# Optimization experiments

Measured on AMD Instinct MI355X. Metric: run time of the kernel, lower is better.

## Reference

```python
import jax, jax.numpy as jnp
import numpy as np

N, E = 50000, 1600000
IN_CH, TOTAL_OUT, HEADS, NUM_LAYERS = 128, 64, 4, 3
C = TOTAL_OUT // HEADS  # out channels per head = 16
NEG_SLOPE = 0.2


def setup_inputs() -> dict:
    key = jax.random.key(0)
    ks = jax.random.split(key, 20)
    inp = {
        'x': jax.random.normal(ks[0], (N, IN_CH), dtype=jnp.float32),
        'edge_index': jax.random.randint(ks[1], (2, E), 0, N, dtype=jnp.int64),
    }
    ki = 2
    for i in range(NUM_LAYERS):
        fan_in = IN_CH if i == 0 else TOTAL_OUT
        s = 1.0 / np.sqrt(fan_in)
        inp[f'W{i}'] = jax.random.uniform(ks[ki], (fan_in, HEADS * C), jnp.float32, -s, s); ki += 1
        inp[f'att_src{i}'] = jax.random.uniform(ks[ki], (HEADS, C), jnp.float32, -s, s); ki += 1
        inp[f'att_dst{i}'] = jax.random.uniform(ks[ki], (HEADS, C), jnp.float32, -s, s); ki += 1
        inp[f'b{i}'] = jnp.zeros((HEADS * C,), dtype=jnp.float32)
    return inp


def gat_layer(x, src, dst, W, att_src, att_dst, b):
    n = x.shape[0]
    h = (x @ W).reshape(n, HEADS, C)                      # [N,H,C]
    a_s = (h * att_src).sum(-1)                            # [N,H]
    a_d = (h * att_dst).sum(-1)                            # [N,H]
    e = jax.nn.leaky_relu(a_s[src] + a_d[dst], NEG_SLOPE)  # [E',H]
    # segment softmax over incoming edges of each dst node
    m = jax.ops.segment_max(e, dst, num_segments=n)        # [N,H]
    ex = jnp.exp(e - m[dst])
    denom = jax.ops.segment_sum(ex, dst, num_segments=n)   # [N,H]
    alpha = ex / (denom[dst] + 1e-16)                      # [E',H]
    out = jax.ops.segment_sum(h[src] * alpha[:, :, None], dst, num_segments=n)  # [N,H,C]
    return out.reshape(n, HEADS * C) + b


def reference(x, edge_index, W0, att_src0, att_dst0, b0,
              W1, att_src1, att_dst1, b1,
              W2, att_src2, att_dst2, b2) -> jnp.ndarray:
    n = x.shape[0]
    loop = jnp.arange(n, dtype=edge_index.dtype)
    src = jnp.concatenate([edge_index[0], loop])  # add_self_loops=True (PyG default)
    dst = jnp.concatenate([edge_index[1], loop])
    params = [(W0, att_src0, att_dst0, b0), (W1, att_src1, att_dst1, b1), (W2, att_src2, att_dst2, b2)]
    h = x
    for i, (W, a_s, a_d, b) in enumerate(params):
        h = gat_layer(h, src, dst, W, a_s, a_d, b)
        if i < NUM_LAYERS - 1:
            h = jax.nn.relu(h)
    return h
```

## Files before the change

### kernel.cpp

```cpp
#include <hip/hip_runtime.h>
#include <hip/hip_fp16.h>
#include <math.h>

#define NN 50000
#define EE 1600000
#define HEADS 4
#define OUTC 64
#define NEG_SLOPE 0.2f

#define BM 64
#define BK 64

#define NB 196
#define RECTOT (EE + NN)
#define PCHUNK 4096
#define SEGCAP 12288
#define BINCAP 9500


__global__ void initcsr_kernel(int* __restrict__ fill1, int* __restrict__ rowptr) {
    int t = threadIdx.x;
    if (t < NB) fill1[t] = 0;
    if (t == 0) rowptr[NN] = RECTOT;
}

__global__ __launch_bounds__(256) void partition_kernel(
        const int* __restrict__ src, const int* __restrict__ dst,
        int* __restrict__ fill1, unsigned* __restrict__ bucket) {
    __shared__ int bh[NB], bbase[NB];
    int t = threadIdx.x;
    if (t < NB) bh[t] = 0;
    __syncthreads();
    int base = blockIdx.x * PCHUNK;
    int dv[16], sv[16], lr[16];
    #pragma unroll
    for (int j = 0; j < 16; ++j) {
        int i = base + j * 256 + t;
        bool valid = i < RECTOT;
        int d = -1, s = 0;
        if (valid) {
            if (i < EE) { d = dst[i]; s = src[i]; }
            else        { d = i - EE; s = d; }
        }
        dv[j] = d; sv[j] = s;
        lr[j] = valid ? atomicAdd(&bh[d >> 8], 1) : 0;
    }
    __syncthreads();
    if (t < NB && bh[t]) bbase[t] = atomicAdd(&fill1[t], bh[t]);
    __syncthreads();
    #pragma unroll
    for (int j = 0; j < 16; ++j) {
        if (dv[j] >= 0) {
            int bin = dv[j] >> 8;
            int pos = bbase[bin] + lr[j];
            if (pos < BINCAP)
                bucket[(size_t)bin * BINCAP + pos] =
                    ((unsigned)(dv[j] & 255) << 16) | (unsigned)sv[j];
        }
    }
}

__global__ void scan_hi_kernel(const int* __restrict__ fill1, int* __restrict__ binStart) {
    int t = threadIdx.x, lane = t & 63, w = t >> 6;
    __shared__ int wsum[4];
    int v = (t < NB) ? fill1[t] : 0;
    int s = v;
    #pragma unroll
    for (int off = 1; off < 64; off <<= 1) {
        int u = __shfl_up(s, off);
        if (lane >= off) s += u;
    }
    if (lane == 63) wsum[w] = s;
    __syncthreads();
    int add = 0;
    for (int i = 0; i < w; ++i) add += wsum[i];
    int excl = add + s - v;
    if (t <= NB) binStart[t] = excl;
}

__global__ __launch_bounds__(256) void seg_sort_kernel(
        const unsigned* __restrict__ bucket, const int* __restrict__ binStart,
        int* __restrict__ rowptr, unsigned short* __restrict__ col) {
    __shared__ unsigned stage[SEGCAP];
    __shared__ int h2[256], b2[256], c2[256];
    __shared__ int wsum[4];
    int t = threadIdx.x, lane = t & 63, w = t >> 6;
    int b = blockIdx.x;
    int segbase = binStart[b], segend = binStart[b + 1];
    int len = segend - segbase;
    const unsigned* __restrict__ bin = bucket + (size_t)b * BINCAP;
    h2[t] = 0; c2[t] = 0;
    __syncthreads();
    for (int i = t; i < len; i += 256) {
        unsigned r = bin[i];
        stage[i] = r;
        atomicAdd(&h2[(r >> 16) & 255], 1);
    }
    __syncthreads();
    int v = h2[t], s = v;
    #pragma unroll
    for (int off = 1; off < 64; off <<= 1) {
        int u = __shfl_up(s, off);
        if (lane >= off) s += u;
    }
    if (lane == 63) wsum[w] = s;
    __syncthreads();
    int add = 0;
    for (int i = 0; i < w; ++i) add += wsum[i];
    int excl = add + s - v;
    b2[t] = excl;
    int d = (b << 8) + t;
    if (d < NN) rowptr[d] = segbase + excl;
    __syncthreads();
    for (int i = t; i < len; i += 256) {
        unsigned r = stage[i];
        int low = (r >> 16) & 255;
        int pos = b2[low] + atomicAdd(&c2[low], 1);
        col[segbase + pos] = (unsigned short)(r & 0xFFFFu);
    }
}

__global__ __launch_bounds__(256) void gemm_att_kernel(
        const float* __restrict__ x, const float* __restrict__ W,
        const float* __restrict__ att_src, const float* __restrict__ att_dst,
        __half* __restrict__ h16,
        float* __restrict__ a_s, float* __restrict__ a_d,
        int n, int K) {
    __shared__ float Xt[BK][BM + 4];
    __shared__ float Ws[BK][OUTC + 4];
    int tid = (int)threadIdx.x;
    int tx = tid & 15, ty = tid >> 4;
    int row0 = blockIdx.x * BM;

    float acc[4][4] = {};

    for (int k0 = 0; k0 < K; k0 += BK) {
        {
            int rb = tid >> 4;
            int kb = tid & 15;
            float4 v0, v1, v2, v3;
            {
                int r0 = row0 + 4 * rb;
                int ra = r0 + 0; if (ra >= n) ra = n - 1;
                int rbx = r0 + 1; if (rbx >= n) rbx = n - 1;
                int rc = r0 + 2; if (rc >= n) rc = n - 1;
                int rd = r0 + 3; if (rd >= n) rd = n - 1;
                const float* xb = x + (size_t)k0 + 4 * kb;
                v0 = *(const float4*)(xb + (size_t)ra * K);
                v1 = *(const float4*)(xb + (size_t)rbx * K);
                v2 = *(const float4*)(xb + (size_t)rc * K);
                v3 = *(const float4*)(xb + (size_t)rd * K);
            }
            *(float4*)&Xt[4 * kb + 0][4 * rb] = make_float4(v0.x, v1.x, v2.x, v3.x);
            *(float4*)&Xt[4 * kb + 1][4 * rb] = make_float4(v0.y, v1.y, v2.y, v3.y);
            *(float4*)&Xt[4 * kb + 2][4 * rb] = make_float4(v0.z, v1.z, v2.z, v3.z);
            *(float4*)&Xt[4 * kb + 3][4 * rb] = make_float4(v0.w, v1.w, v2.w, v3.w);
        }
        {
            int k = tid >> 2;
            int c = (tid & 3) * 16;
            const float4* wp = (const float4*)(W + (size_t)(k0 + k) * OUTC + c);
            float4 v0 = wp[0], v1 = wp[1], v2 = wp[2], v3 = wp[3];
            *(float4*)&Ws[k][c]      = v0;
            *(float4*)&Ws[k][c + 4]  = v1;
            *(float4*)&Ws[k][c + 8]  = v2;
            *(float4*)&Ws[k][c + 12] = v3;
        }
        __syncthreads();
        #pragma unroll 8
        for (int k = 0; k < BK; ++k) {
            float4 xv = *(const float4*)&Xt[k][ty * 4];
            float4 wv = *(const float4*)&Ws[k][tx * 4];
            acc[0][0] = fmaf(xv.x, wv.x, acc[0][0]); acc[0][1] = fmaf(xv.x, wv.y, acc[0][1]);
            acc[0][2] = fmaf(xv.x, wv.z, acc[0][2]); acc[0][3] = fmaf(xv.x, wv.w, acc[0][3]);
            acc[1][0] = fmaf(xv.y, wv.x, acc[1][0]); acc[1][1] = fmaf(xv.y, wv.y, acc[1][1]);
            acc[1][2] = fmaf(xv.y, wv.z, acc[1][2]); acc[1][3] = fmaf(xv.y, wv.w, acc[1][3]);
            acc[2][0] = fmaf(xv.z, wv.x, acc[2][0]); acc[2][1] = fmaf(xv.z, wv.y, acc[2][1]);
            acc[2][2] = fmaf(xv.z, wv.z, acc[2][2]); acc[2][3] = fmaf(xv.z, wv.w, acc[2][3]);
            acc[3][0] = fmaf(xv.w, wv.x, acc[3][0]); acc[3][1] = fmaf(xv.w, wv.y, acc[3][1]);
            acc[3][2] = fmaf(xv.w, wv.z, acc[3][2]); acc[3][3] = fmaf(xv.w, wv.w, acc[3][3]);
        }
        __syncthreads();
    }

    float as0 = att_src[tx * 4 + 0], as1 = att_src[tx * 4 + 1];
    float as2 = att_src[tx * 4 + 2], as3 = att_src[tx * 4 + 3];
    float ad0 = att_dst[tx * 4 + 0], ad1 = att_dst[tx * 4 + 1];
    float ad2 = att_dst[tx * 4 + 2], ad3 = att_dst[tx * 4 + 3];
    int head = tx >> 2;
    #pragma unroll
    for (int i = 0; i < 4; ++i) {
        int row = row0 + ty * 4 + i;
        bool ok = row < n;
        if (ok) {
            union { __half2 h2[2]; uint2 u; } pk;
            pk.h2[0] = __floats2half2_rn(acc[i][0], acc[i][1]);
            pk.h2[1] = __floats2half2_rn(acc[i][2], acc[i][3]);
            *(uint2*)(h16 + (size_t)row * OUTC + tx * 4) = pk.u;
        }
        float ps = acc[i][0] * as0 + acc[i][1] * as1 + acc[i][2] * as2 + acc[i][3] * as3;
        float pd = acc[i][0] * ad0 + acc[i][1] * ad1 + acc[i][2] * ad2 + acc[i][3] * ad3;
        ps += __shfl_xor(ps, 1); ps += __shfl_xor(ps, 2);
        pd += __shfl_xor(pd, 1); pd += __shfl_xor(pd, 2);
        if (ok && (tx & 3) == 0) {
            a_s[row * HEADS + head] = ps;
            a_d[row * HEADS + head] = pd;
        }
    }
}

__global__ __launch_bounds__(256) void gat_aggr16_kernel(
        const int* __restrict__ rowptr, const unsigned short* __restrict__ col,
        const __half* __restrict__ h16, const float* __restrict__ a_s,
        const float* __restrict__ a_d, const float* __restrict__ bias,
        float* __restrict__ out, int n, int do_relu) {
    int node = __builtin_amdgcn_readfirstlane(
        (int)((blockIdx.x * 256u + threadIdx.x) >> 6));
    if (node >= n) return;
    int lane = (int)(threadIdx.x & 63);
    int slot = lane >> 4;
    int cl   = lane & 15;
    int head = cl >> 2;

    int beg = rowptr[node], end = rowptr[node + 1];
    float ad_h = a_d[(node << 2) | head];
    const uint2* __restrict__ hp = (const uint2*)h16;

    float4 acc = make_float4(0.f, 0.f, 0.f, 0.f);
    float den = 0.f;
    int e = beg + slot;
    for (; e + 4 < end; e += 8) {
        int s0 = (int)col[e], s1 = (int)col[e + 4];
        float as0 = a_s[(s0 << 2) | head];
        float as1 = a_s[(s1 << 2) | head];
        uint2 r0 = hp[(s0 << 4) | cl];
        uint2 r1 = hp[(s1 << 4) | cl];
        union { uint2 u; __half2 h2[2]; } p0, p1;
        p0.u = r0; p1.u = r1;
        float2 f00 = __half22float2(p0.h2[0]), f01 = __half22float2(p0.h2[1]);
        float2 f10 = __half22float2(p1.h2[0]), f11 = __half22float2(p1.h2[1]);
        float x0 = as0 + ad_h; x0 = fmaxf(x0, NEG_SLOPE * x0);
        float x1 = as1 + ad_h; x1 = fmaxf(x1, NEG_SLOPE * x1);
        float e0 = __expf(x0), e1 = __expf(x1);
        acc.x = fmaf(e0, f00.x, acc.x); acc.y = fmaf(e0, f00.y, acc.y);
        acc.z = fmaf(e0, f01.x, acc.z); acc.w = fmaf(e0, f01.y, acc.w);
        acc.x = fmaf(e1, f10.x, acc.x); acc.y = fmaf(e1, f10.y, acc.y);
        acc.z = fmaf(e1, f11.x, acc.z); acc.w = fmaf(e1, f11.y, acc.w);
        den += e0 + e1;
    }
    for (; e < end; e += 4) {
        int s0 = (int)col[e];
        float as0 = a_s[(s0 << 2) | head];
        uint2 r0 = hp[(s0 << 4) | cl];
        union { uint2 u; __half2 h2[2]; } p0;
        p0.u = r0;
        float2 f00 = __half22float2(p0.h2[0]), f01 = __half22float2(p0.h2[1]);
        float x0 = as0 + ad_h; x0 = fmaxf(x0, NEG_SLOPE * x0);
        float e0 = __expf(x0);
        acc.x = fmaf(e0, f00.x, acc.x); acc.y = fmaf(e0, f00.y, acc.y);
        acc.z = fmaf(e0, f01.x, acc.z); acc.w = fmaf(e0, f01.y, acc.w);
        den += e0;
    }
    acc.x += __shfl_xor(acc.x, 16); acc.y += __shfl_xor(acc.y, 16);
    acc.z += __shfl_xor(acc.z, 16); acc.w += __shfl_xor(acc.w, 16);
    den   += __shfl_xor(den, 16);
    acc.x += __shfl_xor(acc.x, 32); acc.y += __shfl_xor(acc.y, 32);
    acc.z += __shfl_xor(acc.z, 32); acc.w += __shfl_xor(acc.w, 32);
    den   += __shfl_xor(den, 32);
    if (slot == 0) {
        float inv = 1.0f / (den + 1e-16f);
        float4 bv = ((const float4*)bias)[cl];
        float rx = fmaf(acc.x, inv, bv.x);
        float ry = fmaf(acc.y, inv, bv.y);
        float rz = fmaf(acc.z, inv, bv.z);
        float rw = fmaf(acc.w, inv, bv.w);
        if (do_relu) {
            rx = fmaxf(rx, 0.f); ry = fmaxf(ry, 0.f);
            rz = fmaxf(rz, 0.f); rw = fmaxf(rw, 0.f);
        }
        ((float4*)out)[(node << 4) | cl] = make_float4(rx, ry, rz, rw);
    }
}

extern "C" void kernel_launch(void* const* d_in, const int* in_sizes, int n_in,
                              void* d_out, int out_size, void* d_ws, size_t ws_size,
                              hipStream_t stream) {
    const float* x  = (const float*)d_in[0];
    const int*   ei = (const int*)d_in[1];
    const int*   srcv = ei;
    const int*   dstv = ei + EE;

    const float* W[3]  = { (const float*)d_in[2], (const float*)d_in[6],  (const float*)d_in[10] };
    const float* AS[3] = { (const float*)d_in[3], (const float*)d_in[7],  (const float*)d_in[11] };
    const float* AD[3] = { (const float*)d_in[4], (const float*)d_in[8],  (const float*)d_in[12] };
    const float* B[3]  = { (const float*)d_in[5], (const float*)d_in[9],  (const float*)d_in[13] };

    char* ws = (char*)d_ws;
    size_t off = 0;
    auto carve = [&](size_t bytes) -> char* {
        char* p = ws + off;
        off = (off + bytes + 255) & ~(size_t)255;
        return p;
    };
    int*            rowptr   = (int*)carve((NN + 1) * sizeof(int));
    int*            fill1    = (int*)carve(NB * sizeof(int));
    int*            binStart = (int*)carve((NB + 1) * sizeof(int));
    unsigned short* colv     = (unsigned short*)carve((size_t)RECTOT * sizeof(unsigned short));
    size_t regionA_bytes = (size_t)NB * BINCAP * sizeof(unsigned);
    char*     regionA = carve(regionA_bytes);
    unsigned* bucket  = (unsigned*)regionA;
    __half*   h16     = (__half*)regionA;
    float* xbuf     = (float*)carve((size_t)NN * OUTC * sizeof(float));
    float* a_s      = (float*)carve((size_t)NN * HEADS * sizeof(float));
    float* a_d      = (float*)carve((size_t)NN * HEADS * sizeof(float));

    int pgrid = (RECTOT + PCHUNK - 1) / PCHUNK;
    initcsr_kernel<<<1, 256, 0, stream>>>(fill1, rowptr);
    partition_kernel<<<pgrid, 256, 0, stream>>>(srcv, dstv, fill1, bucket);
    scan_hi_kernel<<<1, 256, 0, stream>>>(fill1, binStart);
    seg_sort_kernel<<<NB, 256, 0, stream>>>(bucket, binStart, rowptr, colv);

    int grid_gemm = (NN + BM - 1) / BM;
    int grid_aggr = (NN + 3) / 4;

    gemm_att_kernel<<<grid_gemm, 256, 0, stream>>>(x, W[0], AS[0], AD[0],
                                                   h16, a_s, a_d, NN, 128);
    gat_aggr16_kernel<<<grid_aggr, 256, 0, stream>>>(rowptr, colv, h16, a_s, a_d, B[0], xbuf, NN, 1);
    gemm_att_kernel<<<grid_gemm, 256, 0, stream>>>(xbuf, W[1], AS[1], AD[1],
                                                   h16, a_s, a_d, NN, 64);
    gat_aggr16_kernel<<<grid_aggr, 256, 0, stream>>>(rowptr, colv, h16, a_s, a_d, B[1], xbuf, NN, 1);
    gemm_att_kernel<<<grid_gemm, 256, 0, stream>>>(xbuf, W[2], AS[2], AD[2],
                                                   h16, a_s, a_d, NN, 64);
    gat_aggr16_kernel<<<grid_aggr, 256, 0, stream>>>(rowptr, colv, h16, a_s, a_d, B[2], (float*)d_out, NN, 0);
}
```

Measured before the change: 212.9 us.

## Co-schedule CSR build with layer-0 GEMM and widen aggregation loads to 16B

The CSR partition and segment-sort kernels now share launches with halves of the layer-0 GEMM, so independent graph-preprocessing and GEMM blocks run concurrently. To allow this, the bucket buffer and h16 no longer alias in workspace. The init kernel becomes a memset, and the rowptr sentinel write moves into the scan. The aggregation kernel now uses 8 lanes per edge with 16-byte loads instead of 16 lanes with 8-byte loads, which processes 8 edges per wave-iteration and adds a third reduction step. The costs are more workspace memory and higher register and shared-memory footprint in the fused kernels.

```diff
diff --git a/kernel.cpp b/kernel.cpp
--- a/kernel.cpp
+++ b/kernel.cpp
@@ -14,24 +14,21 @@
 #define NB 196
 #define RECTOT (EE + NN)
 #define PCHUNK 4096
-#define SEGCAP 12288
+#define PGRID ((RECTOT + PCHUNK - 1) / PCHUNK)
 #define BINCAP 9500
-
-
-__global__ void initcsr_kernel(int* __restrict__ fill1, int* __restrict__ rowptr) {
-    int t = threadIdx.x;
-    if (t < NB) fill1[t] = 0;
-    if (t == 0) rowptr[NN] = RECTOT;
-}
-
-__global__ __launch_bounds__(256) void partition_kernel(
+#define GEMM_BLKS 782
+#define GEMM_A 391
+#define GEMM_B 391
+
+
+__device__ __forceinline__ void partition_body(
+        int* bh, int* bbase, int blk,
         const int* __restrict__ src, const int* __restrict__ dst,
         int* __restrict__ fill1, unsigned* __restrict__ bucket) {
-    __shared__ int bh[NB], bbase[NB];
-    int t = threadIdx.x;
+    int t = (int)threadIdx.x;
     if (t < NB) bh[t] = 0;
     __syncthreads();
-    int base = blockIdx.x * PCHUNK;
+    int base = blk * PCHUNK;
     int dv[16], sv[16], lr[16];
     #pragma unroll
     for (int j = 0; j < 16; ++j) {
@@ -60,32 +57,16 @@
     }
 }
 
-__global__ void scan_hi_kernel(const int* __restrict__ fill1, int* __restrict__ binStart) {
-    int t = threadIdx.x, lane = t & 63, w = t >> 6;
-    __shared__ int wsum[4];
-    int v = (t < NB) ? fill1[t] : 0;
-    int s = v;
-    #pragma unroll
-    for (int off = 1; off < 64; off <<= 1) {
-        int u = __shfl_up(s, off);
-        if (lane >= off) s += u;
-    }
-    if (lane == 63) wsum[w] = s;
-    __syncthreads();
-    int add = 0;
-    for (int i = 0; i < w; ++i) add += wsum[i];
-    int excl = add + s - v;
-    if (t <= NB) binStart[t] = excl;
-}
-
-__global__ __launch_bounds__(256) void seg_sort_kernel(
+__device__ __forceinline__ void seg_sort_body(
+        unsigned char* smem, int b,
         const unsigned* __restrict__ bucket, const int* __restrict__ binStart,
         int* __restrict__ rowptr, unsigned short* __restrict__ col) {
-    __shared__ unsigned stage[SEGCAP];
-    __shared__ int h2[256], b2[256], c2[256];
-    __shared__ int wsum[4];
-    int t = threadIdx.x, lane = t & 63, w = t >> 6;
-    int b = blockIdx.x;
+    unsigned* stage = (unsigned*)smem;
+    int* h2   = (int*)(smem + 38016);
+    int* b2   = h2 + 256;
+    int* c2   = b2 + 256;
+    int* wsum = c2 + 256;
+    int t = (int)threadIdx.x, lane = t & 63, w = t >> 6;
     int segbase = binStart[b], segend = binStart[b + 1];
     int len = segend - segbase;
     const unsigned* __restrict__ bin = bucket + (size_t)b * BINCAP;
@@ -120,17 +101,16 @@
     }
 }
 
-__global__ __launch_bounds__(256) void gemm_att_kernel(
+__device__ __forceinline__ void gemm_body(
+        float (*Xt)[BM + 4], float (*Ws)[OUTC + 4], int gblk,
         const float* __restrict__ x, const float* __restrict__ W,
         const float* __restrict__ att_src, const float* __restrict__ att_dst,
         __half* __restrict__ h16,
         float* __restrict__ a_s, float* __restrict__ a_d,
         int n, int K) {
-    __shared__ float Xt[BK][BM + 4];
-    __shared__ float Ws[BK][OUTC + 4];
     int tid = (int)threadIdx.x;
     int tx = tid & 15, ty = tid >> 4;
-    int row0 = blockIdx.x * BM;
+    int row0 = gblk * BM;
 
     float acc[4][4] = {};
 
@@ -209,6 +189,70 @@
     }
 }
 
+
+__global__ __launch_bounds__(256) void fused_part_gemm(
+        const int* __restrict__ src, const int* __restrict__ dst,
+        int* __restrict__ fill1, unsigned* __restrict__ bucket,
+        const float* __restrict__ x, const float* __restrict__ W,
+        const float* __restrict__ att_src, const float* __restrict__ att_dst,
+        __half* __restrict__ h16, float* __restrict__ a_s, float* __restrict__ a_d,
+        int n, int K) {
+    __shared__ float Xt[BK][BM + 4];
+    __shared__ float Ws[BK][OUTC + 4];
+    __shared__ int bh[NB], bbase[NB];
+    int b = (int)blockIdx.x;
+    if (b < PGRID) partition_body(bh, bbase, b, src, dst, fill1, bucket);
+    else           gemm_body(Xt, Ws, b - PGRID, x, W, att_src, att_dst, h16, a_s, a_d, n, K);
+}
+
+__global__ void scan_hi_kernel(const int* __restrict__ fill1, int* __restrict__ binStart,
+                               int* __restrict__ rowptr) {
+    int t = threadIdx.x, lane = t & 63, w = t >> 6;
+    __shared__ int wsum[4];
+    int v = (t < NB) ? fill1[t] : 0;
+    int s = v;
+    #pragma unroll
+    for (int off = 1; off < 64; off <<= 1) {
+        int u = __shfl_up(s, off);
+        if (lane >= off) s += u;
+    }
+    if (lane == 63) wsum[w] = s;
+    __syncthreads();
+    int add = 0;
+    for (int i = 0; i < w; ++i) add += wsum[i];
+    int excl = add + s - v;
+    if (t <= NB) binStart[t] = excl;
+    if (t == 0) rowptr[NN] = RECTOT;
+}
+
+__global__ __launch_bounds__(256) void fused_sort_gemm(
+        const unsigned* __restrict__ bucket, const int* __restrict__ binStart,
+        int* __restrict__ rowptr, unsigned short* __restrict__ col,
+        const float* __restrict__ x, const float* __restrict__ W,
+        const float* __restrict__ att_src, const float* __restrict__ att_dst,
+        __half* __restrict__ h16, float* __restrict__ a_s, float* __restrict__ a_d,
+        int n, int K) {
+    __shared__ __align__(16) unsigned char smem[41216];
+    int b = (int)blockIdx.x;
+    if (b < NB) {
+        seg_sort_body(smem, b, bucket, binStart, rowptr, col);
+    } else {
+        float (*Xt)[BM + 4]   = (float(*)[BM + 4])smem;
+        float (*Ws)[OUTC + 4] = (float(*)[OUTC + 4])(smem + sizeof(float) * BK * (BM + 4));
+        gemm_body(Xt, Ws, GEMM_A + (b - NB), x, W, att_src, att_dst, h16, a_s, a_d, n, K);
+    }
+}
+
+__global__ __launch_bounds__(256) void gemm_att_kernel(
+        const float* __restrict__ x, const float* __restrict__ W,
+        const float* __restrict__ att_src, const float* __restrict__ att_dst,
+        __half* __restrict__ h16, float* __restrict__ a_s, float* __restrict__ a_d,
+        int n, int K) {
+    __shared__ float Xt[BK][BM + 4];
+    __shared__ float Ws[BK][OUTC + 4];
+    gemm_body(Xt, Ws, (int)blockIdx.x, x, W, att_src, att_dst, h16, a_s, a_d, n, K);
+}
+
 __global__ __launch_bounds__(256) void gat_aggr16_kernel(
         const int* __restrict__ rowptr, const unsigned short* __restrict__ col,
         const __half* __restrict__ h16, const float* __restrict__ a_s,
@@ -218,67 +262,79 @@
         (int)((blockIdx.x * 256u + threadIdx.x) >> 6));
     if (node >= n) return;
     int lane = (int)(threadIdx.x & 63);
-    int slot = lane >> 4;
-    int cl   = lane & 15;
-    int head = cl >> 2;
+    int slot = lane >> 3;
+    int cl   = lane & 7;
+    int head = cl >> 1;
 
     int beg = rowptr[node], end = rowptr[node + 1];
     float ad_h = a_d[(node << 2) | head];
-    const uint2* __restrict__ hp = (const uint2*)h16;
-
-    float4 acc = make_float4(0.f, 0.f, 0.f, 0.f);
+    const uint4* __restrict__ hp = (const uint4*)h16;
+
+    float4 a0 = make_float4(0.f, 0.f, 0.f, 0.f);
+    float4 a1 = make_float4(0.f, 0.f, 0.f, 0.f);
     float den = 0.f;
     int e = beg + slot;
-    for (; e + 4 < end; e += 8) {
-        int s0 = (int)col[e], s1 = (int)col[e + 4];
+    for (; e + 8 < end; e += 16) {
+        int s0 = (int)col[e], s1 = (int)col[e + 8];
         float as0 = a_s[(s0 << 2) | head];
         float as1 = a_s[(s1 << 2) | head];
-        uint2 r0 = hp[(s0 << 4) | cl];
-        uint2 r1 = hp[(s1 << 4) | cl];
-        union { uint2 u; __half2 h2[2]; } p0, p1;
-        p0.u = r0; p1.u = r1;
-        float2 f00 = __half22float2(p0.h2[0]), f01 = __half22float2(p0.h2[1]);
-        float2 f10 = __half22float2(p1.h2[0]), f11 = __half22float2(p1.h2[1]);
+        uint4 r0 = hp[(s0 << 3) | cl];
+        uint4 r1 = hp[(s1 << 3) | cl];
         float x0 = as0 + ad_h; x0 = fmaxf(x0, NEG_SLOPE * x0);
         float x1 = as1 + ad_h; x1 = fmaxf(x1, NEG_SLOPE * x1);
         float e0 = __expf(x0), e1 = __expf(x1);
-        acc.x = fmaf(e0, f00.x, acc.x); acc.y = fmaf(e0, f00.y, acc.y);
-        acc.z = fmaf(e0, f01.x, acc.z); acc.w = fmaf(e0, f01.y, acc.w);
-        acc.x = fmaf(e1, f10.x, acc.x); acc.y = fmaf(e1, f10.y, acc.y);
-        acc.z = fmaf(e1, f11.x, acc.z); acc.w = fmaf(e1, f11.y, acc.w);
+        union { uint4 u; __half2 h2[4]; } p0, p1;
+        p0.u = r0; p1.u = r1;
+        float2 f;
+        f = __half22float2(p0.h2[0]); a0.x = fmaf(e0, f.x, a0.x); a0.y = fmaf(e0, f.y, a0.y);
+        f = __half22float2(p0.h2[1]); a0.z = fmaf(e0, f.x, a0.z); a0.w = fmaf(e0, f.y, a0.w);
+        f = __half22float2(p0.h2[2]); a1.x = fmaf(e0, f.x, a1.x); a1.y = fmaf(e0, f.y, a1.y);
+        f = __half22float2(p0.h2[3]); a1.z = fmaf(e0, f.x, a1.z); a1.w = fmaf(e0, f.y, a1.w);
+        f = __half22float2(p1.h2[0]); a0.x = fmaf(e1, f.x, a0.x); a0.y = fmaf(e1, f.y, a0.y);
+        f = __half22float2(p1.h2[1]); a0.z = fmaf(e1, f.x, a0.z); a0.w = fmaf(e1, f.y, a0.w);
+        f = __half22float2(p1.h2[2]); a1.x = fmaf(e1, f.x, a1.x); a1.y = fmaf(e1, f.y, a1.y);
+        f = __half22float2(p1.h2[3]); a1.z = fmaf(e1, f.x, a1.z); a1.w = fmaf(e1, f.y, a1.w);
         den += e0 + e1;
     }
-    for (; e < end; e += 4) {
+    for (; e < end; e += 8) {
         int s0 = (int)col[e];
         float as0 = a_s[(s0 << 2) | head];
-        uint2 r0 = hp[(s0 << 4) | cl];
-        union { uint2 u; __half2 h2[2]; } p0;
-        p0.u = r0;
-        float2 f00 = __half22float2(p0.h2[0]), f01 = __half22float2(p0.h2[1]);
+        uint4 r0 = hp[(s0 << 3) | cl];
         float x0 = as0 + ad_h; x0 = fmaxf(x0, NEG_SLOPE * x0);
         float e0 = __expf(x0);
-        acc.x = fmaf(e0, f00.x, acc.x); acc.y = fmaf(e0, f00.y, acc.y);
-        acc.z = fmaf(e0, f01.x, acc.z); acc.w = fmaf(e0, f01.y, acc.w);
+        union { uint4 u; __half2 h2[4]; } p0;
+        p0.u = r0;
+        float2 f;
+        f = __half22float2(p0.h2[0]); a0.x = fmaf(e0, f.x, a0.x); a0.y = fmaf(e0, f.y, a0.y);
+        f = __half22float2(p0.h2[1]); a0.z = fmaf(e0, f.x, a0.z); a0.w = fmaf(e0, f.y, a0.w);
+        f = __half22float2(p0.h2[2]); a1.x = fmaf(e0, f.x, a1.x); a1.y = fmaf(e0, f.y, a1.y);
+        f = __half22float2(p0.h2[3]); a1.z = fmaf(e0, f.x, a1.z); a1.w = fmaf(e0, f.y, a1.w);
         den += e0;
     }
-    acc.x += __shfl_xor(acc.x, 16); acc.y += __shfl_xor(acc.y, 16);
-    acc.z += __shfl_xor(acc.z, 16); acc.w += __shfl_xor(acc.w, 16);
-    den   += __shfl_xor(den, 16);
-    acc.x += __shfl_xor(acc.x, 32); acc.y += __shfl_xor(acc.y, 32);
-    acc.z += __shfl_xor(acc.z, 32); acc.w += __shfl_xor(acc.w, 32);
-    den   += __shfl_xor(den, 32);
+    #pragma unroll
+    for (int off = 8; off <= 32; off <<= 1) {
+        a0.x += __shfl_xor(a0.x, off); a0.y += __shfl_xor(a0.y, off);
+        a0.z += __shfl_xor(a0.z, off); a0.w += __shfl_xor(a0.w, off);
+        a1.x += __shfl_xor(a1.x, off); a1.y += __shfl_xor(a1.y, off);
+        a1.z += __shfl_xor(a1.z, off); a1.w += __shfl_xor(a1.w, off);
+        den  += __shfl_xor(den, off);
+    }
     if (slot == 0) {
         float inv = 1.0f / (den + 1e-16f);
-        float4 bv = ((const float4*)bias)[cl];
-        float rx = fmaf(acc.x, inv, bv.x);
-        float ry = fmaf(acc.y, inv, bv.y);
-        float rz = fmaf(acc.z, inv, bv.z);
-        float rw = fmaf(acc.w, inv, bv.w);
+        float4 b0 = ((const float4*)bias)[cl * 2];
+        float4 b1 = ((const float4*)bias)[cl * 2 + 1];
+        float4 r0 = make_float4(fmaf(a0.x, inv, b0.x), fmaf(a0.y, inv, b0.y),
+                                fmaf(a0.z, inv, b0.z), fmaf(a0.w, inv, b0.w));
+        float4 r1 = make_float4(fmaf(a1.x, inv, b1.x), fmaf(a1.y, inv, b1.y),
+                                fmaf(a1.z, inv, b1.z), fmaf(a1.w, inv, b1.w));
         if (do_relu) {
-            rx = fmaxf(rx, 0.f); ry = fmaxf(ry, 0.f);
-            rz = fmaxf(rz, 0.f); rw = fmaxf(rw, 0.f);
-        }
-        ((float4*)out)[(node << 4) | cl] = make_float4(rx, ry, rz, rw);
+            r0.x = fmaxf(r0.x, 0.f); r0.y = fmaxf(r0.y, 0.f);
+            r0.z = fmaxf(r0.z, 0.f); r0.w = fmaxf(r0.w, 0.f);
+            r1.x = fmaxf(r1.x, 0.f); r1.y = fmaxf(r1.y, 0.f);
+            r1.z = fmaxf(r1.z, 0.f); r1.w = fmaxf(r1.w, 0.f);
+        }
+        ((float4*)out)[(node << 4) | (cl << 1)]       = r0;
+        ((float4*)out)[((node << 4) | (cl << 1)) + 1] = r1;
     }
 }
 
@@ -306,30 +362,26 @@
     int*            fill1    = (int*)carve(NB * sizeof(int));
     int*            binStart = (int*)carve((NB + 1) * sizeof(int));
     unsigned short* colv     = (unsigned short*)carve((size_t)RECTOT * sizeof(unsigned short));
-    size_t regionA_bytes = (size_t)NB * BINCAP * sizeof(unsigned);
-    char*     regionA = carve(regionA_bytes);
-    unsigned* bucket  = (unsigned*)regionA;
-    __half*   h16     = (__half*)regionA;
+    unsigned* bucket = (unsigned*)carve((size_t)NB * BINCAP * sizeof(unsigned));
+    __half*   h16    = (__half*)carve((size_t)NN * OUTC * sizeof(__half));
     float* xbuf     = (float*)carve((size_t)NN * OUTC * sizeof(float));
     float* a_s      = (float*)carve((size_t)NN * HEADS * sizeof(float));
     float* a_d      = (float*)carve((size_t)NN * HEADS * sizeof(float));
 
-    int pgrid = (RECTOT + PCHUNK - 1) / PCHUNK;
-    initcsr_kernel<<<1, 256, 0, stream>>>(fill1, rowptr);
-    partition_kernel<<<pgrid, 256, 0, stream>>>(srcv, dstv, fill1, bucket);
-    scan_hi_kernel<<<1, 256, 0, stream>>>(fill1, binStart);
-    seg_sort_kernel<<<NB, 256, 0, stream>>>(bucket, binStart, rowptr, colv);
-
-    int grid_gemm = (NN + BM - 1) / BM;
     int grid_aggr = (NN + 3) / 4;
 
-    gemm_att_kernel<<<grid_gemm, 256, 0, stream>>>(x, W[0], AS[0], AD[0],
-                                                   h16, a_s, a_d, NN, 128);
+    hipMemsetAsync(fill1, 0, NB * sizeof(int), stream);
+    fused_part_gemm<<<PGRID + GEMM_A, 256, 0, stream>>>(
+        srcv, dstv, fill1, bucket,
+        x, W[0], AS[0], AD[0], h16, a_s, a_d, NN, 128);
+    scan_hi_kernel<<<1, 256, 0, stream>>>(fill1, binStart, rowptr);
+    fused_sort_gemm<<<NB + GEMM_B, 256, 0, stream>>>(
+        bucket, binStart, rowptr, colv,
+        x, W[0], AS[0], AD[0], h16, a_s, a_d, NN, 128);
+
     gat_aggr16_kernel<<<grid_aggr, 256, 0, stream>>>(rowptr, colv, h16, a_s, a_d, B[0], xbuf, NN, 1);
-    gemm_att_kernel<<<grid_gemm, 256, 0, stream>>>(xbuf, W[1], AS[1], AD[1],
-                                                   h16, a_s, a_d, NN, 64);
+    gemm_att_kernel<<<GEMM_BLKS, 256, 0, stream>>>(xbuf, W[1], AS[1], AD[1], h16, a_s, a_d, NN, 64);
     gat_aggr16_kernel<<<grid_aggr, 256, 0, stream>>>(rowptr, colv, h16, a_s, a_d, B[1], xbuf, NN, 1);
-    gemm_att_kernel<<<grid_gemm, 256, 0, stream>>>(xbuf, W[2], AS[2], AD[2],
-                                                   h16, a_s, a_d, NN, 64);
+    gemm_att_kernel<<<GEMM_BLKS, 256, 0, stream>>>(xbuf, W[2], AS[2], AD[2], h16, a_s, a_d, NN, 64);
     gat_aggr16_kernel<<<grid_aggr, 256, 0, stream>>>(rowptr, colv, h16, a_s, a_d, B[2], (float*)d_out, NN, 0);
 }
```

Result: faster. 179.1 us (-15.9%).
